# Optimization experiments

Measured on AMD Instinct MI355X. Metric: run time of the kernel, lower is better.

## Reference

```python
import jax, jax.numpy as jnp
import numpy as np

B, C, H, W = 2, 32, 256, 1216
PT = 6
EPS = 1e-6

def _conv(x, w):
    # 3x3 conv, stride 1, SAME padding, NCHW/OIHW
    return jax.lax.conv_general_dilated(x, w, (1, 1), ((1, 1), (1, 1)),
                                        dimension_numbers=('NCHW', 'OIHW', 'NCHW'))

def _cbn(x, w, s, b):
    # conv (bias=False) + eval-mode BatchNorm folded into per-channel scale/bias
    return _conv(x, w) * s[None, :, None, None] + b[None, :, None, None]

def _cb(x, w, b):
    # conv with bias (no norm branch of Basic2d)
    return _conv(x, w) + b[None, :, None, None]

def _gen_kernel(fout, w1, s1, b1, w2, s2, b2):
    # GenKernel: normalized per-pixel kernel with middle weight = 1 - sum(others)
    h = jax.nn.relu(_cbn(fout, w1, s1, b1))
    w = _cbn(h, w2, s2, b2)  # [B, pk*pk-1, H, W]
    w = w / (jnp.sum(jnp.abs(w), axis=1, keepdims=True) + EPS)
    wmid = 1.0 - jnp.sum(w, axis=1, keepdims=True)
    half = w.shape[1] // 2
    return jnp.concatenate([w[:, :half], wmid, w[:, half:]], axis=1)  # [B, pk*pk, H, W]

def _local_conv(x, w, k):
    # bpconvlocal: per-pixel spatially-varying k x k convolution of a 1-channel map
    p = k // 2
    _, _, Hx, Wx = x.shape
    xp = jnp.pad(x, ((0, 0), (0, 0), (p, p), (p, p)))
    patches = jnp.stack([xp[:, 0, i:i + Hx, j:j + Wx]
                         for i in range(k) for j in range(k)], axis=1)  # [B, k*k, H, W]
    return jnp.sum(w * patches, axis=1, keepdims=True)

def _cspn(fout, hn, h0,
          k3w1, k3s1, k3b1, k3w2, k3s2, k3b2,
          k5w1, k5s1, k5b1, k5w2, k5s2, k5b2,
          k7w1, k7s1, k7b1, k7w2, k7s2, k7b2,
          mw1, ms1, mb1, mw2, mbias2,
          cw1, cs1, cb1, cw2, cbias2,
          tw1, ts1, tb1, tw2, tbias2):
    w3 = _gen_kernel(fout, k3w1, k3s1, k3b1, k3w2, k3s2, k3b2)
    w5 = _gen_kernel(fout, k5w1, k5s1, k5b1, k5w2, k5s2, k5b2)
    w7 = _gen_kernel(fout, k7w1, k7s1, k7b1, k7w2, k7s2, k7b2)
    valid = (h0 > 0.001).astype(fout.dtype)
    mask = jax.nn.sigmoid(_cb(jax.nn.relu(_cbn(fout, mw1, ms1, mb1)), mw2, mbias2)) * valid
    m3, m5, m7 = jnp.split(mask, 3, axis=1)
    conf = jax.nn.softmax(_cb(jax.nn.relu(_cbn(fout, cw1, cs1, cb1)), cw2, cbias2), axis=1)
    c3, c5, c7 = jnp.split(conf, 3, axis=1)
    h3 = h5 = h7 = hn
    hns = [hn]
    for i in range(PT):
        h3 = (1.0 - m3) * _local_conv(h3, w3, 3) + m3 * h0
        h5 = (1.0 - m5) * _local_conv(h5, w5, 5) + m5 * h0
        h7 = (1.0 - m7) * _local_conv(h7, w7, 7) + m7 * h0
        if i == PT // 2 - 1:
            hns.append(c3 * h3 + c5 * h5 + c7 * h7)
    hns.append(c3 * h3 + c5 * h5 + c7 * h7)
    hns = jnp.concatenate(hns, axis=1)  # [B, 3, H, W]
    wt = jax.nn.softmax(_cb(jax.nn.relu(_cbn(jnp.concatenate([fout, hns], axis=1),
                                             tw1, ts1, tb1)), tw2, tbias2), axis=1)
    return jnp.sum(wt * hns, axis=1, keepdims=True)

def setup_inputs():
    key = jax.random.key(0)
    ks = iter(jax.random.split(key, 80))
    def nrm(shape, s=0.05):
        return jax.random.normal(next(ks), shape, dtype=jnp.float32) * s
    d = {}
    d['fout'] = jax.random.normal(next(ks), (B, C, H, W), dtype=jnp.float32)
    d['hn'] = jax.random.uniform(next(ks), (B, 1, H, W), dtype=jnp.float32) * 10.0
    sparse = (jax.random.uniform(next(ks), (B, 1, H, W)) < 0.06).astype(jnp.float32)
    d['h0'] = sparse * jax.random.uniform(next(ks), (B, 1, H, W), dtype=jnp.float32) * 10.0
    for pk, pre in ((3, 'k3'), (5, 'k5'), (7, 'k7')):
        co = pk * pk - 1
        d[pre + 'w1'] = nrm((C, C, 3, 3)); d[pre + 's1'] = 1.0 + nrm((C,)); d[pre + 'b1'] = nrm((C,))
        d[pre + 'w2'] = nrm((co, C, 3, 3)); d[pre + 's2'] = 1.0 + nrm((co,)); d[pre + 'b2'] = nrm((co,))
    for pre, cin in (('m', C), ('c', C), ('t', C + 3)):
        d[pre + 'w1'] = nrm((C, cin, 3, 3)); d[pre + 's1'] = 1.0 + nrm((C,)); d[pre + 'b1'] = nrm((C,))
        d[pre + 'w2'] = nrm((3, C, 3, 3)); d[pre + 'bias2'] = nrm((3,))
    return d

def reference(fout, hn, h0,
              k3w1, k3s1, k3b1, k3w2, k3s2, k3b2,
              k5w1, k5s1, k5b1, k5w2, k5s2, k5b2,
              k7w1, k7s1, k7b1, k7w2, k7s2, k7b2,
              mw1, ms1, mb1, mw2, mbias2,
              cw1, cs1, cb1, cw2, cbias2,
              tw1, ts1, tb1, tw2, tbias2):
    return _cspn(fout, hn, h0,
                 k3w1, k3s1, k3b1, k3w2, k3s2, k3b2,
                 k5w1, k5s1, k5b1, k5w2, k5s2, k5b2,
                 k7w1, k7s1, k7b1, k7w2, k7s2, k7b2,
                 mw1, ms1, mb1, mw2, mbias2,
                 cw1, cs1, cb1, cw2, cbias2,
                 tw1, ts1, tb1, tw2, tbias2)
```

## Files before the change

kernel.cpp:

```cpp
#include <hip/hip_runtime.h>
#include <hip/hip_bf16.h>

constexpr int B_ = 2, H_ = 256, W_ = 1216;
constexpr int HW = H_ * W_;
constexpr int NP = B_ * HW;
constexpr int WP = W_ + 2;
constexpr int HP = H_ + 2;
constexpr int HWP = HP * WP;
constexpr float EPS_ = 1e-6f;

constexpr int PW1_K3 = 0;
constexpr int PW1_K5 = 18432;
constexpr int PW1_K7 = 36864;
constexpr int PW2_K3 = 55296;
constexpr int PW2_K5 = 64512;
constexpr int PW2_K7 = 82944;
constexpr int PP1_M  = 110592;
constexpr int PP1_C  = 119808;
constexpr int PP1_T  = 129024;
constexpr int PP1T2  = 138240;
constexpr int PG2_M  = 140544;
constexpr int PG2_C  = 145152;
constexpr int PG2_T  = 149760;
constexpr int PREP_N = 154368;

typedef __bf16 bfrag __attribute__((ext_vector_type(8)));
typedef float f4 __attribute__((ext_vector_type(4)));

union BU { uint4 u; bfrag f; };
union U8 { uint4 u; ushort s[8]; };

__device__ __forceinline__ ushort f2b(float x) {
  uint u = __float_as_uint(x);
  u += 0x7fffu + ((u >> 16) & 1u);
  return (ushort)(u >> 16);
}
__device__ __forceinline__ float b2f(ushort u) {
  return __uint_as_float(((uint)u) << 16);
}

__global__ __launch_bounds__(256)
void prep_k(const float* __restrict__ k3w1, const float* __restrict__ k5w1,
            const float* __restrict__ k7w1, const float* __restrict__ k3w2,
            const float* __restrict__ k5w2, const float* __restrict__ k7w2,
            const float* __restrict__ mw1, const float* __restrict__ cw1,
            const float* __restrict__ tw1, const float* __restrict__ mw2,
            const float* __restrict__ cw2, const float* __restrict__ tw2,
            ushort* __restrict__ wp)
{
  int i = blockIdx.x * 256 + threadIdx.x;
  if (i >= PREP_N) return;
  ushort outv;
  if (i < PW2_K3) {
    int c = i / 18432, r = i % 18432;
    const float* src = (c == 0) ? k3w1 : (c == 1) ? k5w1 : k7w1;
    int ci = r & 31; int t1 = r >> 5;
    int co = t1 & 31; int t2 = t1 >> 5;
    int tap = t2 % 9, half = t2 / 9;
    float v = src[(co * 32 + ci) * 9 + tap];
    ushort hi = f2b(v);
    outv = half ? f2b(v - b2f(hi)) : hi;
  } else if (i < PP1_M) {
    int r = i - PW2_K3;
    const float* src; int NM16, CO;
    if (r < 9216)       { src = k3w2; NM16 = 16; CO = 8; }
    else if (r < 27648) { src = k5w2; NM16 = 32; CO = 24; r -= 9216; }
    else                { src = k7w2; NM16 = 48; CO = 48; r -= 27648; }
    int ci = r & 31; int t1 = r >> 5;
    int co = t1 % NM16; int t2 = t1 / NM16;
    int tap = t2 % 9, half = t2 / 9;
    if (co < CO) {
      float v = src[(co * 32 + ci) * 9 + tap];
      ushort hi = f2b(v);
      outv = half ? f2b(v - b2f(hi)) : hi;
    } else outv = 0;
  } else if (i < PP1T2) {
    int r = i - PP1_M;
    int c = r / 9216; r %= 9216;
    const float* src = (c == 0) ? mw1 : (c == 1) ? cw1 : tw1;
    int CIN = (c == 2) ? 35 : 32;
    int ci = r & 31; int t1 = r >> 5;
    int co = t1 & 31, tap = t1 >> 5;
    outv = f2b(src[(co * CIN + ci) * 9 + tap]);
  } else if (i < PG2_M) {
    int r = i - PP1T2;
    int c8 = r & 7; int t1 = r >> 3;
    int co = t1 & 31, tap = t1 >> 5;
    int cc = (c8 < 3) ? c8 : ((c8 < 6) ? c8 - 3 : -1);
    outv = (cc >= 0) ? f2b(tw1[(co * 35 + 32 + cc) * 9 + tap]) : (ushort)0;
  } else {
    int r = i - PG2_M;
    int c = r / 4608; r %= 4608;
    const float* src = (c == 0) ? mw2 : (c == 1) ? cw2 : tw2;
    int ci = r & 31; int t1 = r >> 5;
    int co = t1 & 15, tap = t1 >> 4;
    outv = (co < 3) ? f2b(src[(co * 32 + ci) * 9 + tap]) : (ushort)0;
  }
  wp[i] = outv;
}

__global__ __launch_bounds__(256)
void zring_k(ushort* __restrict__ hP) {
  constexpr int PB = 2 * WP * 4 + 2 * (HP - 2) * 4;
  int i = blockIdx.x * 256 + threadIdx.x;
  if (i >= 2 * PB) return;
  int b = i / PB, r = i % PB;
  size_t idx;
  if (r < WP * 4) idx = (size_t)r;
  else if (r < 2 * WP * 4) idx = (size_t)(HP - 1) * WP * 4 + (r - WP * 4);
  else {
    int q = r - 2 * WP * 4;
    int row = q >> 3, k = q & 7;
    int col = (k < 4) ? k : (WP - 1) * 4 + (k - 4);
    idx = (size_t)(row + 1) * WP * 4 + col;
  }
  *(uint4*)&hP[(size_t)b * HWP * 32 + idx * 8] = uint4{0, 0, 0, 0};
}

__global__ __launch_bounds__(256, 3)
void convs1(const float* __restrict__ xf, const ushort* __restrict__ wp,
            const float* __restrict__ scale, const float* __restrict__ bias,
            ushort* __restrict__ outh)
{
  __shared__ ushort xl[25344];

  const int tid = threadIdx.x;
  const int lane = tid & 63;
  const int wid = tid >> 6;
  const int x0 = blockIdx.x * 64, y0 = blockIdx.y * 4, b = blockIdx.z;

  for (int i = tid; i < 396 * 4; i += 256) {
    int oct = i & 3, rest = i >> 2;
    int xx = rest % 66, rr = rest / 66;
    int yy = y0 - 1 + rr, x = x0 - 1 + xx;
    uint4 vh = {0, 0, 0, 0}, vl = {0, 0, 0, 0};
    if ((unsigned)yy < (unsigned)H_ && (unsigned)x < (unsigned)W_) {
      const float* src = xf + ((size_t)b * 32 + oct * 8) * HW + (size_t)yy * W_ + x;
      uint uh[4], ul[4];
#pragma unroll
      for (int j = 0; j < 4; ++j) {
        float a = src[(size_t)(2 * j + 0) * HW];
        float c = src[(size_t)(2 * j + 1) * HW];
        ushort ah = f2b(a), ch = f2b(c);
        ushort al = f2b(a - b2f(ah)), cl = f2b(c - b2f(ch));
        uh[j] = (uint)ah | ((uint)ch << 16);
        ul[j] = (uint)al | ((uint)cl << 16);
      }
      vh = uint4{uh[0], uh[1], uh[2], uh[3]};
      vl = uint4{ul[0], ul[1], ul[2], ul[3]};
    }
    *(uint4*)&xl[rest * 32 + oct * 8] = vh;
    *(uint4*)&xl[12672 + rest * 32 + oct * 8] = vl;
  }
  __syncthreads();

  const int n = lane & 15, quad = lane >> 4;

  f4 acc[4][2];
#pragma unroll
  for (int tu = 0; tu < 4; ++tu)
#pragma unroll
    for (int mt = 0; mt < 2; ++mt) acc[tu][mt] = f4{0.f, 0.f, 0.f, 0.f};

#pragma unroll
  for (int tap = 0; tap < 9; ++tap) {
    int dy = tap / 3, dx = tap % 3;
    bfrag avhi[2], avlo[2];
#pragma unroll
    for (int mt = 0; mt < 2; ++mt) {
      avhi[mt] = *(const bfrag*)&wp[((tap * 32) + mt * 16 + n) * 32 + quad * 8];
      avlo[mt] = *(const bfrag*)&wp[(((9 + tap) * 32) + mt * 16 + n) * 32 + quad * 8];
    }
#pragma unroll
    for (int tu = 0; tu < 4; ++tu) {
      int t = wid + tu * 4;
      int r = t >> 2, g = t & 3;
      int pix = (r + dy) * 66 + g * 16 + n + dx;
      bfrag bhi = *(const bfrag*)&xl[pix * 32 + quad * 8];
      bfrag blo = *(const bfrag*)&xl[12672 + pix * 32 + quad * 8];
#pragma unroll
      for (int mt = 0; mt < 2; ++mt) {
        acc[tu][mt] = __builtin_amdgcn_mfma_f32_16x16x32_bf16(avhi[mt], bhi, acc[tu][mt], 0, 0, 0);
        acc[tu][mt] = __builtin_amdgcn_mfma_f32_16x16x32_bf16(avhi[mt], blo, acc[tu][mt], 0, 0, 0);
        acc[tu][mt] = __builtin_amdgcn_mfma_f32_16x16x32_bf16(avlo[mt], bhi, acc[tu][mt], 0, 0, 0);
      }
    }
  }

#pragma unroll
  for (int tu = 0; tu < 4; ++tu) {
    int t = wid + tu * 4;
    int r = t >> 2, g = t & 3;
    int gx = x0 + g * 16 + n, gy = y0 + r;
    size_t bpix = (size_t)b * HWP + (size_t)(gy + 1) * WP + (gx + 1);
#pragma unroll
    for (int mt = 0; mt < 2; ++mt) {
      int cob = mt * 16 + quad * 4;
      float v0 = fmaxf(acc[tu][mt][0] * scale[cob + 0] + bias[cob + 0], 0.f);
      float v1 = fmaxf(acc[tu][mt][1] * scale[cob + 1] + bias[cob + 1], 0.f);
      float v2 = fmaxf(acc[tu][mt][2] * scale[cob + 2] + bias[cob + 2], 0.f);
      float v3 = fmaxf(acc[tu][mt][3] * scale[cob + 3] + bias[cob + 3], 0.f);
      uint u0 = (uint)f2b(v0) | ((uint)f2b(v1) << 16);
      uint u1 = (uint)f2b(v2) | ((uint)f2b(v3) << 16);
      *(uint2*)&outh[bpix * 32 + cob] = uint2{u0, u1};
    }
  }
}

template<int nM, int MINW>
__global__ __launch_bounds__(256, MINW)
void convs2(const ushort* __restrict__ hP, const ushort* __restrict__ wp,
            const float* __restrict__ scale, const float* __restrict__ bias,
            ushort* __restrict__ outw, int CO)
{
  __shared__ ushort xl[12672];

  constexpr int NM16 = nM * 16;
  const int tid = threadIdx.x;
  const int lane = tid & 63;
  const int wid = tid >> 6;
  const int x0 = blockIdx.x * 64, y0 = blockIdx.y * 4, b = blockIdx.z;
  const ushort* hb = hP + (size_t)b * HWP * 32;

  for (int i = tid; i < 396 * 4; i += 256) {
    int oct = i & 3, rest = i >> 2;
    int xx = rest % 66, rr = rest / 66;
    *(uint4*)&xl[rest * 32 + oct * 8] =
        *(const uint4*)&hb[((size_t)(y0 + rr) * WP + (x0 + xx)) * 32 + oct * 8];
  }

  const int n = lane & 15, quad = lane >> 4;

  f4 acc[4][nM];
#pragma unroll
  for (int tu = 0; tu < 4; ++tu)
#pragma unroll
    for (int mt = 0; mt < nM; ++mt) acc[tu][mt] = f4{0.f, 0.f, 0.f, 0.f};

  bfrag whi[2][nM], wlo[2][nM];
#pragma unroll
  for (int mt = 0; mt < nM; ++mt) {
    whi[0][mt] = *(const bfrag*)&wp[(mt * 16 + n) * 32 + quad * 8];
    wlo[0][mt] = *(const bfrag*)&wp[((9 * NM16) + mt * 16 + n) * 32 + quad * 8];
  }
  __syncthreads();

#pragma unroll
  for (int tap = 0; tap < 9; ++tap) {
    const int dy = tap / 3, dx = tap % 3;
    const int cur = tap & 1, nxt = cur ^ 1;
    if (tap < 8) {
#pragma unroll
      for (int mt = 0; mt < nM; ++mt) {
        whi[nxt][mt] = *(const bfrag*)&wp[(((tap + 1) * NM16) + mt * 16 + n) * 32 + quad * 8];
        wlo[nxt][mt] = *(const bfrag*)&wp[(((9 + tap + 1) * NM16) + mt * 16 + n) * 32 + quad * 8];
      }
    }
#pragma unroll
    for (int tu = 0; tu < 4; ++tu) {
      int t = wid + tu * 4;
      int r = t >> 2, g = t & 3;
      int pix = (r + dy) * 66 + g * 16 + n + dx;
      bfrag bv = *(const bfrag*)&xl[pix * 32 + quad * 8];
#pragma unroll
      for (int mt = 0; mt < nM; ++mt) {
        acc[tu][mt] = __builtin_amdgcn_mfma_f32_16x16x32_bf16(whi[cur][mt], bv, acc[tu][mt], 0, 0, 0);
        acc[tu][mt] = __builtin_amdgcn_mfma_f32_16x16x32_bf16(wlo[cur][mt], bv, acc[tu][mt], 0, 0, 0);
      }
    }
  }

#pragma unroll
  for (int tu = 0; tu < 4; ++tu) {
    int t = wid + tu * 4;
    int r = t >> 2, g = t & 3;
    int gx = x0 + g * 16 + n, gy = y0 + r;
    size_t gpix = (size_t)gy * W_ + gx;

    float vs[nM][4];
    float pa = 0.f;
#pragma unroll
    for (int mt = 0; mt < nM; ++mt)
#pragma unroll
      for (int rg = 0; rg < 4; ++rg) {
        int co = mt * 16 + quad * 4 + rg;
        float v = (co < CO) ? acc[tu][mt][rg] * scale[co] + bias[co] : 0.f;
        vs[mt][rg] = v;
        pa += fabsf(v);
      }
    pa += __shfl_xor(pa, 16);
    pa += __shfl_xor(pa, 32);
    float inv = 1.f / (pa + EPS_);

    size_t base = ((size_t)b * HW + gpix) * (size_t)CO;
#pragma unroll
    for (int mt = 0; mt < nM; ++mt) {
      int cob = mt * 16 + quad * 4;
      if (cob < CO) {
        uint u0 = (uint)f2b(vs[mt][0] * inv) | ((uint)f2b(vs[mt][1] * inv) << 16);
        uint u1 = (uint)f2b(vs[mt][2] * inv) | ((uint)f2b(vs[mt][3] * inv) << 16);
        *(uint2*)&outw[base + cob] = uint2{u0, u1};
      }
    }
  }
}

template<int KB2, int MINW>
__global__ __launch_bounds__(256, MINW)
void conv1p(const float* __restrict__ xf, const float* __restrict__ hnsp,
            const ushort* __restrict__ wp, const ushort* __restrict__ wp2,
            const float* __restrict__ scale, const float* __restrict__ bias,
            ushort* __restrict__ outh)
{
  __shared__ ushort xl[396 * 32];
  __shared__ ushort xl2[KB2 ? 396 * 8 : 8];

  const int tid = threadIdx.x;
  const int lane = tid & 63;
  const int wid = tid >> 6;
  const int x0 = blockIdx.x * 64, y0 = blockIdx.y * 4, b = blockIdx.z;

  if (KB2) {
    for (int i = tid; i < 396; i += 256) {
      int xx = i % 66, rr = i / 66;
      int yy = y0 - 1 + rr, x = x0 - 1 + xx;
      float v0 = 0.f, v1 = 0.f, v2 = 0.f;
      if ((unsigned)yy < (unsigned)H_ && (unsigned)x < (unsigned)W_) {
        size_t pix = (size_t)yy * W_ + x;
        v0 = hnsp[((size_t)b * 3 + 0) * HW + pix];
        v1 = hnsp[((size_t)b * 3 + 1) * HW + pix];
        v2 = hnsp[((size_t)b * 3 + 2) * HW + pix];
      }
      ushort h0b = f2b(v0), h1b = f2b(v1), h2b = f2b(v2);
      ushort l0 = f2b(v0 - b2f(h0b)), l1 = f2b(v1 - b2f(h1b)), l2 = f2b(v2 - b2f(h2b));
      uint u0 = (uint)h0b | ((uint)h1b << 16);
      uint u1 = (uint)h2b | ((uint)l0 << 16);
      uint u2 = (uint)l1 | ((uint)l2 << 16);
      *(uint4*)&xl2[i * 8] = uint4{u0, u1, u2, 0};
    }
  }
  for (int i = tid; i < 396 * 4; i += 256) {
    int oct = i & 3, rest = i >> 2;
    int xx = rest % 66, rr = rest / 66;
    int yy = y0 - 1 + rr, x = x0 - 1 + xx;
    uint4 v = {0, 0, 0, 0};
    if ((unsigned)yy < (unsigned)H_ && (unsigned)x < (unsigned)W_) {
      const float* src = xf + ((size_t)b * 32 + oct * 8) * HW + (size_t)yy * W_ + x;
      uint u[4];
#pragma unroll
      for (int j = 0; j < 4; ++j) {
        float a = src[(size_t)(2 * j + 0) * HW];
        float c = src[(size_t)(2 * j + 1) * HW];
        u[j] = (uint)f2b(a) | ((uint)f2b(c) << 16);
      }
      v = uint4{u[0], u[1], u[2], u[3]};
    }
    *(uint4*)&xl[rest * 32 + oct * 8] = v;
  }
  __syncthreads();

  const int n = lane & 15, quad = lane >> 4;

  f4 acc[4][2];
#pragma unroll
  for (int tu = 0; tu < 4; ++tu)
#pragma unroll
    for (int mt = 0; mt < 2; ++mt) acc[tu][mt] = f4{0.f, 0.f, 0.f, 0.f};

#pragma unroll
  for (int tap = 0; tap < 9; ++tap) {
    int dy = tap / 3, dx = tap % 3;
    bfrag av[2];
#pragma unroll
    for (int mt = 0; mt < 2; ++mt)
      av[mt] = *(const bfrag*)&wp[((tap * 32) + mt * 16 + n) * 32 + quad * 8];
    bfrag a2[KB2 ? 2 : 1];
    if (KB2) {
#pragma unroll
      for (int mt = 0; mt < 2; ++mt) {
        BU t; t.u = uint4{0, 0, 0, 0};
        if (lane < 16) t.f = *(const bfrag*)&wp2[(tap * 32 + mt * 16 + lane) * 8];
        a2[mt] = t.f;
      }
    }
#pragma unroll
    for (int tu = 0; tu < 4; ++tu) {
      int t = wid + tu * 4;
      int r = t >> 2, g = t & 3;
      int pix = (r + dy) * 66 + g * 16 + n + dx;
      bfrag bv = *(const bfrag*)&xl[pix * 32 + quad * 8];
#pragma unroll
      for (int mt = 0; mt < 2; ++mt)
        acc[tu][mt] = __builtin_amdgcn_mfma_f32_16x16x32_bf16(av[mt], bv, acc[tu][mt], 0, 0, 0);
      if (KB2) {
        BU t2; t2.u = uint4{0, 0, 0, 0};
        if (lane < 16) t2.f = *(const bfrag*)&xl2[pix * 8];
#pragma unroll
        for (int mt = 0; mt < 2; ++mt)
          acc[tu][mt] = __builtin_amdgcn_mfma_f32_16x16x32_bf16(a2[mt], t2.f, acc[tu][mt], 0, 0, 0);
      }
    }
  }

#pragma unroll
  for (int tu = 0; tu < 4; ++tu) {
    int t = wid + tu * 4;
    int r = t >> 2, g = t & 3;
    int gx = x0 + g * 16 + n, gy = y0 + r;
    size_t bpix = (size_t)b * HWP + (size_t)(gy + 1) * WP + (gx + 1);
#pragma unroll
    for (int mt = 0; mt < 2; ++mt) {
      int cob = mt * 16 + quad * 4;
      float v0 = fmaxf(acc[tu][mt][0] * scale[cob + 0] + bias[cob + 0], 0.f);
      float v1 = fmaxf(acc[tu][mt][1] * scale[cob + 1] + bias[cob + 1], 0.f);
      float v2 = fmaxf(acc[tu][mt][2] * scale[cob + 2] + bias[cob + 2], 0.f);
      float v3 = fmaxf(acc[tu][mt][3] * scale[cob + 3] + bias[cob + 3], 0.f);
      uint u0 = (uint)f2b(v0) | ((uint)f2b(v1) << 16);
      uint u1 = (uint)f2b(v2) | ((uint)f2b(v3) << 16);
      *(uint2*)&outh[bpix * 32 + cob] = uint2{u0, u1};
    }
  }
}

template<int EPI>
__global__ __launch_bounds__(256, 4)
void conv2g(const ushort* __restrict__ hP, const ushort* __restrict__ wp,
            const float* __restrict__ bias, const float* __restrict__ h0,
            const float* __restrict__ hnsp, float* __restrict__ outf)
{
  __shared__ ushort xl[12672];

  const int tid = threadIdx.x;
  const int lane = tid & 63;
  const int wid = tid >> 6;
  const int x0 = blockIdx.x * 64, y0 = blockIdx.y * 4, b = blockIdx.z;
  const int n = lane & 15, quad = lane >> 4;
  const ushort* hb = hP + (size_t)b * HWP * 32;

  for (int i = tid; i < 396 * 4; i += 256) {
    int oct = i & 3, rest = i >> 2;
    int xx = rest % 66, rr = rest / 66;
    *(uint4*)&xl[rest * 32 + oct * 8] =
        *(const uint4*)&hb[((size_t)(y0 + rr) * WP + (x0 + xx)) * 32 + oct * 8];
  }

  bfrag av[9];
#pragma unroll
  for (int tap = 0; tap < 9; ++tap)
    av[tap] = *(const bfrag*)&wp[((tap * 16) + n) * 32 + quad * 8];

  f4 acc[4];
#pragma unroll
  for (int tu = 0; tu < 4; ++tu) acc[tu] = f4{0.f, 0.f, 0.f, 0.f};
  __syncthreads();

#pragma unroll
  for (int tap = 0; tap < 9; ++tap) {
    int dy = tap / 3, dx = tap % 3;
#pragma unroll
    for (int tu = 0; tu < 4; ++tu) {
      int t = wid + tu * 4;
      int r = t >> 2, g = t & 3;
      int pix = (r + dy) * 66 + g * 16 + n + dx;
      bfrag bv = *(const bfrag*)&xl[pix * 32 + quad * 8];
      acc[tu] = __builtin_amdgcn_mfma_f32_16x16x32_bf16(av[tap], bv, acc[tu], 0, 0, 0);
    }
  }

#pragma unroll
  for (int tu = 0; tu < 4; ++tu) {
    int t = wid + tu * 4;
    int r = t >> 2, g = t & 3;
    int gx = x0 + g * 16 + n, gy = y0 + r;
    size_t gpix = (size_t)gy * W_ + gx;
    size_t bpix = (size_t)b * HW + gpix;

    if constexpr (EPI == 2) {
      if (lane < 16) {
        float valid = (h0[bpix] > 0.001f) ? 1.f : 0.f;
#pragma unroll
        for (int rg = 0; rg < 3; ++rg) {
          float v = acc[tu][rg] + bias[rg];
          float sg = 1.f / (1.f + expf(-v));
          outf[((size_t)b * 3 + rg) * HW + gpix] = sg * valid;
        }
      }
    } else if constexpr (EPI == 3) {
      if (lane < 16) {
        float v0 = acc[tu][0] + bias[0];
        float v1 = acc[tu][1] + bias[1];
        float v2 = acc[tu][2] + bias[2];
        float m = fmaxf(v0, fmaxf(v1, v2));
        float e0 = expf(v0 - m), e1 = expf(v1 - m), e2 = expf(v2 - m);
        float inv = 1.f / (e0 + e1 + e2);
        outf[((size_t)b * 3 + 0) * HW + gpix] = e0 * inv;
        outf[((size_t)b * 3 + 1) * HW + gpix] = e1 * inv;
        outf[((size_t)b * 3 + 2) * HW + gpix] = e2 * inv;
      }
    } else if constexpr (EPI == 4) {
      if (lane < 16) {
        float v0 = acc[tu][0] + bias[0];
        float v1 = acc[tu][1] + bias[1];
        float v2 = acc[tu][2] + bias[2];
        float m = fmaxf(v0, fmaxf(v1, v2));
        float e0 = expf(v0 - m), e1 = expf(v1 - m), e2 = expf(v2 - m);
        float inv = 1.f / (e0 + e1 + e2);
        float a0 = hnsp[((size_t)b * 3 + 0) * HW + gpix];
        float a1 = hnsp[((size_t)b * 3 + 1) * HW + gpix];
        float a2v = hnsp[((size_t)b * 3 + 2) * HW + gpix];
        outf[bpix] = (e0 * a0 + e1 * a1 + e2 * a2v) * inv;
      }
    }
  }
}

__global__ __launch_bounds__(256)
void init_k(const float* __restrict__ hn, float* __restrict__ h3,
            float* __restrict__ h5, float* __restrict__ h7,
            float* __restrict__ hns)
{
  int t = blockIdx.x * 256 + threadIdx.x;
  if (t >= NP) return;
  float v = hn[t];
  h3[t] = v; h5[t] = v; h7[t] = v;
  int b = t / HW, rem = t - b * HW;
  hns[(size_t)b * 3 * HW + rem] = v;
}

__global__ __launch_bounds__(256)
void iterate_k(const float* __restrict__ h3i, const float* __restrict__ h5i,
               const float* __restrict__ h7i,
               float* __restrict__ h3o, float* __restrict__ h5o,
               float* __restrict__ h7o,
               const ushort* __restrict__ w3, const ushort* __restrict__ w5,
               const ushort* __restrict__ w7,
               const float* __restrict__ mask, const float* __restrict__ h0,
               float* __restrict__ hns, int chn, const float* __restrict__ conf)
{
  int t = blockIdx.x * 256 + threadIdx.x;
  if (t >= NP) return;
  int b = t / HW;
  int rem = t - b * HW;
  int y = rem / W_;
  int x = rem - y * W_;
  size_t pb = (size_t)b * HW;

  float h0v = h0[t];

  U8 a3; a3.u = *(const uint4*)&w3[((size_t)b * HW + rem) * 8];
  float s3 = 0.f, ws3 = 0.f;
#pragma unroll
  for (int p = 0; p < 8; ++p) {
    int tap = (p < 4) ? p : p + 1;
    int dy = tap / 3 - 1, dx = tap % 3 - 1;
    int yy = y + dy, xx = x + dx;
    float hv = ((unsigned)yy < (unsigned)H_ && (unsigned)xx < (unsigned)W_)
                   ? h3i[pb + yy * W_ + xx] : 0.f;
    float wv = b2f(a3.s[p]);
    ws3 += wv;
    s3 += wv * hv;
  }
  s3 += (1.f - ws3) * h3i[t];
  float m3 = mask[(size_t)(b * 3 + 0) * HW + rem];
  float n3 = (1.f - m3) * s3 + m3 * h0v;
  h3o[t] = n3;

  U8 a5[3];
  {
    const ushort* w5r = w5 + ((size_t)b * HW + rem) * 24;
#pragma unroll
    for (int q = 0; q < 3; ++q) a5[q].u = *(const uint4*)(w5r + q * 8);
  }
  float s5 = 0.f, ws5 = 0.f;
#pragma unroll
  for (int p = 0; p < 24; ++p) {
    int tap = (p < 12) ? p : p + 1;
    int dy = tap / 5 - 2, dx = tap % 5 - 2;
    int yy = y + dy, xx = x + dx;
    float hv = ((unsigned)yy < (unsigned)H_ && (unsigned)xx < (unsigned)W_)
                   ? h5i[pb + yy * W_ + xx] : 0.f;
    float wv = b2f(a5[p >> 3].s[p & 7]);
    ws5 += wv;
    s5 += wv * hv;
  }
  s5 += (1.f - ws5) * h5i[t];
  float m5 = mask[(size_t)(b * 3 + 1) * HW + rem];
  float n5 = (1.f - m5) * s5 + m5 * h0v;
  h5o[t] = n5;

  U8 a7[6];
  {
    const ushort* w7r = w7 + ((size_t)b * HW + rem) * 48;
#pragma unroll
    for (int q = 0; q < 6; ++q) a7[q].u = *(const uint4*)(w7r + q * 8);
  }
  float s7 = 0.f, ws7 = 0.f;
#pragma unroll
  for (int p = 0; p < 48; ++p) {
    int tap = (p < 24) ? p : p + 1;
    int dy = tap / 7 - 3, dx = tap % 7 - 3;
    int yy = y + dy, xx = x + dx;
    float hv = ((unsigned)yy < (unsigned)H_ && (unsigned)xx < (unsigned)W_)
                   ? h7i[pb + yy * W_ + xx] : 0.f;
    float wv = b2f(a7[p >> 3].s[p & 7]);
    ws7 += wv;
    s7 += wv * hv;
  }
  s7 += (1.f - ws7) * h7i[t];
  float m7 = mask[(size_t)(b * 3 + 2) * HW + rem];
  float n7 = (1.f - m7) * s7 + m7 * h0v;
  h7o[t] = n7;

  if (chn >= 0) {
    float c3 = conf[(size_t)(b * 3 + 0) * HW + rem];
    float c5 = conf[(size_t)(b * 3 + 1) * HW + rem];
    float c7 = conf[(size_t)(b * 3 + 2) * HW + rem];
    hns[(size_t)(b * 3 + chn) * HW + rem] = c3 * n3 + c5 * n5 + c7 * n7;
  }
}

extern "C" void kernel_launch(void* const* d_in, const int* in_sizes, int n_in,
                              void* d_out, int out_size, void* d_ws, size_t ws_size,
                              hipStream_t stream) {
  const float* fout = (const float*)d_in[0];
  const float* hn   = (const float*)d_in[1];
  const float* h0   = (const float*)d_in[2];
  const float* k3w1 = (const float*)d_in[3];
  const float* k3s1 = (const float*)d_in[4];
  const float* k3b1 = (const float*)d_in[5];
  const float* k3w2 = (const float*)d_in[6];
  const float* k3s2 = (const float*)d_in[7];
  const float* k3b2 = (const float*)d_in[8];
  const float* k5w1 = (const float*)d_in[9];
  const float* k5s1 = (const float*)d_in[10];
  const float* k5b1 = (const float*)d_in[11];
  const float* k5w2 = (const float*)d_in[12];
  const float* k5s2 = (const float*)d_in[13];
  const float* k5b2 = (const float*)d_in[14];
  const float* k7w1 = (const float*)d_in[15];
  const float* k7s1 = (const float*)d_in[16];
  const float* k7b1 = (const float*)d_in[17];
  const float* k7w2 = (const float*)d_in[18];
  const float* k7s2 = (const float*)d_in[19];
  const float* k7b2 = (const float*)d_in[20];
  const float* mw1  = (const float*)d_in[21];
  const float* ms1  = (const float*)d_in[22];
  const float* mb1  = (const float*)d_in[23];
  const float* mw2  = (const float*)d_in[24];
  const float* mbias2 = (const float*)d_in[25];
  const float* cw1  = (const float*)d_in[26];
  const float* cs1  = (const float*)d_in[27];
  const float* cb1  = (const float*)d_in[28];
  const float* cw2  = (const float*)d_in[29];
  const float* cbias2 = (const float*)d_in[30];
  const float* tw1  = (const float*)d_in[31];
  const float* ts1  = (const float*)d_in[32];
  const float* tb1  = (const float*)d_in[33];
  const float* tw2  = (const float*)d_in[34];
  const float* tbias2 = (const float*)d_in[35];

  float* out = (float*)d_out;

  size_t hP_elems = (size_t)2 * HWP * 32;
  size_t need = hP_elems * 2 + (size_t)NP * (80 * 2 + 15 * 4) + (size_t)PREP_N * 2;
  if (ws_size < need) return;
  ushort* hPb  = (ushort*)d_ws;
  ushort* w3   = hPb  + hP_elems;
  ushort* w5   = w3   + (size_t)8 * NP;
  ushort* w7   = w5   + (size_t)24 * NP;
  float* mask  = (float*)(w7 + (size_t)48 * NP);
  float* conf  = mask + (size_t)3 * NP;
  float* hA    = conf + (size_t)3 * NP;
  float* hns   = hA   + (size_t)6 * NP;
  ushort* wp   = (ushort*)(hns + (size_t)3 * NP);

  dim3 blk(256);
  dim3 gc(W_ / 64, H_ / 4, B_);
  int ge = NP / 256;
  constexpr int PB = 2 * WP * 4 + 2 * (HP - 2) * 4;
  int gz = (2 * PB + 255) / 256;
  int gp = (PREP_N + 255) / 256;

  prep_k<<<gp, blk, 0, stream>>>(k3w1, k5w1, k7w1, k3w2, k5w2, k7w2,
                                 mw1, cw1, tw1, mw2, cw2, tw2, wp);
  zring_k<<<gz, blk, 0, stream>>>(hPb);

  convs1<<<gc, blk, 0, stream>>>(fout, wp + PW1_K3, k3s1, k3b1, hPb);
  convs2<1, 4><<<gc, blk, 0, stream>>>(hPb, wp + PW2_K3, k3s2, k3b2, w3, 8);
  convs1<<<gc, blk, 0, stream>>>(fout, wp + PW1_K5, k5s1, k5b1, hPb);
  convs2<2, 4><<<gc, blk, 0, stream>>>(hPb, wp + PW2_K5, k5s2, k5b2, w5, 24);
  convs1<<<gc, blk, 0, stream>>>(fout, wp + PW1_K7, k7s1, k7b1, hPb);
  convs2<3, 3><<<gc, blk, 0, stream>>>(hPb, wp + PW2_K7, k7s2, k7b2, w7, 48);

  conv1p<0, 4><<<gc, blk, 0, stream>>>(fout, nullptr, wp + PP1_M, nullptr, ms1, mb1, hPb);
  conv2g<2><<<gc, blk, 0, stream>>>(hPb, wp + PG2_M, mbias2, h0, nullptr, mask);

  conv1p<0, 4><<<gc, blk, 0, stream>>>(fout, nullptr, wp + PP1_C, nullptr, cs1, cb1, hPb);
  conv2g<3><<<gc, blk, 0, stream>>>(hPb, wp + PG2_C, cbias2, nullptr, nullptr, conf);

  float* h3c = hA + (size_t)0 * NP; float* h3n = hA + (size_t)1 * NP;
  float* h5c = hA + (size_t)2 * NP; float* h5n = hA + (size_t)3 * NP;
  float* h7c = hA + (size_t)4 * NP; float* h7n = hA + (size_t)5 * NP;

  init_k<<<ge, blk, 0, stream>>>(hn, h3c, h5c, h7c, hns);
  for (int i = 0; i < 6; ++i) {
    int chn = (i == 2) ? 1 : ((i == 5) ? 2 : -1);
    iterate_k<<<ge, blk, 0, stream>>>(h3c, h5c, h7c, h3n, h5n, h7n,
                                      w3, w5, w7, mask, h0, hns, chn, conf);
    float* t;
    t = h3c; h3c = h3n; h3n = t;
    t = h5c; h5c = h5n; h5n = t;
    t = h7c; h7c = h7n; h7n = t;
  }

  conv1p<1, 3><<<gc, blk, 0, stream>>>(fout, hns, wp + PP1_T, wp + PP1T2, ts1, tb1, hPb);
  conv2g<4><<<gc, blk, 0, stream>>>(hPb, wp + PG2_T, tbias2, nullptr, hns, out);
}
```

Before: 899.2 us.

## Fuse first-layer convs of kernel and mask/conf branches sharing one input tile

```diff
diff --git a/kernel.cpp b/kernel.cpp
--- a/kernel.cpp
+++ b/kernel.cpp
@@ -103,8 +103,8 @@
 void zring_k(ushort* __restrict__ hP) {
   constexpr int PB = 2 * WP * 4 + 2 * (HP - 2) * 4;
   int i = blockIdx.x * 256 + threadIdx.x;
-  if (i >= 2 * PB) return;
-  int b = i / PB, r = i % PB;
+  if (i >= 6 * PB) return;
+  int bp = i / PB, r = i % PB;
   size_t idx;
   if (r < WP * 4) idx = (size_t)r;
   else if (r < 2 * WP * 4) idx = (size_t)(HP - 1) * WP * 4 + (r - WP * 4);
@@ -114,13 +114,15 @@
     int col = (k < 4) ? k : (WP - 1) * 4 + (k - 4);
     idx = (size_t)(row + 1) * WP * 4 + col;
   }
-  *(uint4*)&hP[(size_t)b * HWP * 32 + idx * 8] = uint4{0, 0, 0, 0};
+  *(uint4*)&hP[(size_t)bp * HWP * 32 + idx * 8] = uint4{0, 0, 0, 0};
 }
 
 __global__ __launch_bounds__(256, 3)
-void convs1(const float* __restrict__ xf, const ushort* __restrict__ wp,
-            const float* __restrict__ scale, const float* __restrict__ bias,
-            ushort* __restrict__ outh)
+void convs1f(const float* __restrict__ xf, const ushort* __restrict__ wp,
+             const float* __restrict__ s3, const float* __restrict__ b3,
+             const float* __restrict__ s5, const float* __restrict__ b5,
+             const float* __restrict__ s7, const float* __restrict__ b7,
+             ushort* __restrict__ outh)
 {
   __shared__ ushort xl[25344];
 
@@ -156,53 +158,165 @@
 
   const int n = lane & 15, quad = lane >> 4;
 
-  f4 acc[4][2];
-#pragma unroll
-  for (int tu = 0; tu < 4; ++tu)
-#pragma unroll
-    for (int mt = 0; mt < 2; ++mt) acc[tu][mt] = f4{0.f, 0.f, 0.f, 0.f};
-
-#pragma unroll
-  for (int tap = 0; tap < 9; ++tap) {
-    int dy = tap / 3, dx = tap % 3;
-    bfrag avhi[2], avlo[2];
+#pragma unroll 1
+  for (int br = 0; br < 3; ++br) {
+    const ushort* wb = wp + br * 18432;
+    const float* scale = (br == 0) ? s3 : (br == 1) ? s5 : s7;
+    const float* bias  = (br == 0) ? b3 : (br == 1) ? b5 : b7;
+    ushort* ob = outh + (size_t)br * 2 * HWP * 32;
+
+    f4 acc[4][2];
+#pragma unroll
+    for (int tu = 0; tu < 4; ++tu)
+#pragma unroll
+      for (int mt = 0; mt < 2; ++mt) acc[tu][mt] = f4{0.f, 0.f, 0.f, 0.f};
+
+    bfrag avhi[2][2], avlo[2][2];
 #pragma unroll
     for (int mt = 0; mt < 2; ++mt) {
-      avhi[mt] = *(const bfrag*)&wp[((tap * 32) + mt * 16 + n) * 32 + quad * 8];
-      avlo[mt] = *(const bfrag*)&wp[(((9 + tap) * 32) + mt * 16 + n) * 32 + quad * 8];
-    }
+      avhi[0][mt] = *(const bfrag*)&wb[(mt * 16 + n) * 32 + quad * 8];
+      avlo[0][mt] = *(const bfrag*)&wb[((9 * 32) + mt * 16 + n) * 32 + quad * 8];
+    }
+
+#pragma unroll
+    for (int tap = 0; tap < 9; ++tap) {
+      const int dy = tap / 3, dx = tap % 3;
+      const int cur = tap & 1, nxt = cur ^ 1;
+      if (tap < 8) {
+#pragma unroll
+        for (int mt = 0; mt < 2; ++mt) {
+          avhi[nxt][mt] = *(const bfrag*)&wb[(((tap + 1) * 32) + mt * 16 + n) * 32 + quad * 8];
+          avlo[nxt][mt] = *(const bfrag*)&wb[(((9 + tap + 1) * 32) + mt * 16 + n) * 32 + quad * 8];
+        }
+      }
+#pragma unroll
+      for (int tu = 0; tu < 4; ++tu) {
+        int t = wid + tu * 4;
+        int r = t >> 2, g = t & 3;
+        int pix = (r + dy) * 66 + g * 16 + n + dx;
+        bfrag bhi = *(const bfrag*)&xl[pix * 32 + quad * 8];
+        bfrag blo = *(const bfrag*)&xl[12672 + pix * 32 + quad * 8];
+#pragma unroll
+        for (int mt = 0; mt < 2; ++mt) {
+          acc[tu][mt] = __builtin_amdgcn_mfma_f32_16x16x32_bf16(avhi[cur][mt], bhi, acc[tu][mt], 0, 0, 0);
+          acc[tu][mt] = __builtin_amdgcn_mfma_f32_16x16x32_bf16(avhi[cur][mt], blo, acc[tu][mt], 0, 0, 0);
+          acc[tu][mt] = __builtin_amdgcn_mfma_f32_16x16x32_bf16(avlo[cur][mt], bhi, acc[tu][mt], 0, 0, 0);
+        }
+      }
+    }
+
 #pragma unroll
     for (int tu = 0; tu < 4; ++tu) {
       int t = wid + tu * 4;
       int r = t >> 2, g = t & 3;
-      int pix = (r + dy) * 66 + g * 16 + n + dx;
-      bfrag bhi = *(const bfrag*)&xl[pix * 32 + quad * 8];
-      bfrag blo = *(const bfrag*)&xl[12672 + pix * 32 + quad * 8];
+      int gx = x0 + g * 16 + n, gy = y0 + r;
+      size_t bpix = (size_t)b * HWP + (size_t)(gy + 1) * WP + (gx + 1);
 #pragma unroll
       for (int mt = 0; mt < 2; ++mt) {
-        acc[tu][mt] = __builtin_amdgcn_mfma_f32_16x16x32_bf16(avhi[mt], bhi, acc[tu][mt], 0, 0, 0);
-        acc[tu][mt] = __builtin_amdgcn_mfma_f32_16x16x32_bf16(avhi[mt], blo, acc[tu][mt], 0, 0, 0);
-        acc[tu][mt] = __builtin_amdgcn_mfma_f32_16x16x32_bf16(avlo[mt], bhi, acc[tu][mt], 0, 0, 0);
-      }
-    }
-  }
-
-#pragma unroll
-  for (int tu = 0; tu < 4; ++tu) {
-    int t = wid + tu * 4;
-    int r = t >> 2, g = t & 3;
-    int gx = x0 + g * 16 + n, gy = y0 + r;
-    size_t bpix = (size_t)b * HWP + (size_t)(gy + 1) * WP + (gx + 1);
-#pragma unroll
-    for (int mt = 0; mt < 2; ++mt) {
-      int cob = mt * 16 + quad * 4;
-      float v0 = fmaxf(acc[tu][mt][0] * scale[cob + 0] + bias[cob + 0], 0.f);
-      float v1 = fmaxf(acc[tu][mt][1] * scale[cob + 1] + bias[cob + 1], 0.f);
-      float v2 = fmaxf(acc[tu][mt][2] * scale[cob + 2] + bias[cob + 2], 0.f);
-      float v3 = fmaxf(acc[tu][mt][3] * scale[cob + 3] + bias[cob + 3], 0.f);
-      uint u0 = (uint)f2b(v0) | ((uint)f2b(v1) << 16);
-      uint u1 = (uint)f2b(v2) | ((uint)f2b(v3) << 16);
-      *(uint2*)&outh[bpix * 32 + cob] = uint2{u0, u1};
+        int cob = mt * 16 + quad * 4;
+        float v0 = fmaxf(acc[tu][mt][0] * scale[cob + 0] + bias[cob + 0], 0.f);
+        float v1 = fmaxf(acc[tu][mt][1] * scale[cob + 1] + bias[cob + 1], 0.f);
+        float v2 = fmaxf(acc[tu][mt][2] * scale[cob + 2] + bias[cob + 2], 0.f);
+        float v3 = fmaxf(acc[tu][mt][3] * scale[cob + 3] + bias[cob + 3], 0.f);
+        uint u0 = (uint)f2b(v0) | ((uint)f2b(v1) << 16);
+        uint u1 = (uint)f2b(v2) | ((uint)f2b(v3) << 16);
+        *(uint2*)&ob[bpix * 32 + cob] = uint2{u0, u1};
+      }
+    }
+  }
+}
+
+__global__ __launch_bounds__(256, 4)
+void conv1pf(const float* __restrict__ xf, const ushort* __restrict__ wp,
+             const float* __restrict__ sm, const float* __restrict__ bm,
+             const float* __restrict__ sc, const float* __restrict__ bc,
+             ushort* __restrict__ outh)
+{
+  __shared__ ushort xl[12672];
+
+  const int tid = threadIdx.x;
+  const int lane = tid & 63;
+  const int wid = tid >> 6;
+  const int x0 = blockIdx.x * 64, y0 = blockIdx.y * 4, b = blockIdx.z;
+
+  for (int i = tid; i < 396 * 4; i += 256) {
+    int oct = i & 3, rest = i >> 2;
+    int xx = rest % 66, rr = rest / 66;
+    int yy = y0 - 1 + rr, x = x0 - 1 + xx;
+    uint4 v = {0, 0, 0, 0};
+    if ((unsigned)yy < (unsigned)H_ && (unsigned)x < (unsigned)W_) {
+      const float* src = xf + ((size_t)b * 32 + oct * 8) * HW + (size_t)yy * W_ + x;
+      uint u[4];
+#pragma unroll
+      for (int j = 0; j < 4; ++j) {
+        float a = src[(size_t)(2 * j + 0) * HW];
+        float c = src[(size_t)(2 * j + 1) * HW];
+        u[j] = (uint)f2b(a) | ((uint)f2b(c) << 16);
+      }
+      v = uint4{u[0], u[1], u[2], u[3]};
+    }
+    *(uint4*)&xl[rest * 32 + oct * 8] = v;
+  }
+  __syncthreads();
+
+  const int n = lane & 15, quad = lane >> 4;
+
+#pragma unroll 1
+  for (int br = 0; br < 2; ++br) {
+    const ushort* wb = wp + br * 9216;
+    const float* scale = br ? sc : sm;
+    const float* bias  = br ? bc : bm;
+    ushort* ob = outh + (size_t)br * 2 * HWP * 32;
+
+    f4 acc[4][2];
+#pragma unroll
+    for (int tu = 0; tu < 4; ++tu)
+#pragma unroll
+      for (int mt = 0; mt < 2; ++mt) acc[tu][mt] = f4{0.f, 0.f, 0.f, 0.f};
+
+    bfrag av[2][2];
+#pragma unroll
+    for (int mt = 0; mt < 2; ++mt)
+      av[0][mt] = *(const bfrag*)&wb[(mt * 16 + n) * 32 + quad * 8];
+
+#pragma unroll
+    for (int tap = 0; tap < 9; ++tap) {
+      const int dy = tap / 3, dx = tap % 3;
+      const int cur = tap & 1, nxt = cur ^ 1;
+      if (tap < 8) {
+#pragma unroll
+        for (int mt = 0; mt < 2; ++mt)
+          av[nxt][mt] = *(const bfrag*)&wb[(((tap + 1) * 32) + mt * 16 + n) * 32 + quad * 8];
+      }
+#pragma unroll
+      for (int tu = 0; tu < 4; ++tu) {
+        int t = wid + tu * 4;
+        int r = t >> 2, g = t & 3;
+        int pix = (r + dy) * 66 + g * 16 + n + dx;
+        bfrag bv = *(const bfrag*)&xl[pix * 32 + quad * 8];
+#pragma unroll
+        for (int mt = 0; mt < 2; ++mt)
+          acc[tu][mt] = __builtin_amdgcn_mfma_f32_16x16x32_bf16(av[cur][mt], bv, acc[tu][mt], 0, 0, 0);
+      }
+    }
+
+#pragma unroll
+    for (int tu = 0; tu < 4; ++tu) {
+      int t = wid + tu * 4;
+      int r = t >> 2, g = t & 3;
+      int gx = x0 + g * 16 + n, gy = y0 + r;
+      size_t bpix = (size_t)b * HWP + (size_t)(gy + 1) * WP + (gx + 1);
+#pragma unroll
+      for (int mt = 0; mt < 2; ++mt) {
+        int cob = mt * 16 + quad * 4;
+        float v0 = fmaxf(acc[tu][mt][0] * scale[cob + 0] + bias[cob + 0], 0.f);
+        float v1 = fmaxf(acc[tu][mt][1] * scale[cob + 1] + bias[cob + 1], 0.f);
+        float v2 = fmaxf(acc[tu][mt][2] * scale[cob + 2] + bias[cob + 2], 0.f);
+        float v3 = fmaxf(acc[tu][mt][3] * scale[cob + 3] + bias[cob + 3], 0.f);
+        uint u0 = (uint)f2b(v0) | ((uint)f2b(v1) << 16);
+        uint u1 = (uint)f2b(v2) | ((uint)f2b(v3) << 16);
+        *(uint2*)&ob[bpix * 32 + cob] = uint2{u0, u1};
+      }
     }
   }
 }
@@ -662,10 +776,10 @@
   float* out = (float*)d_out;
 
   size_t hP_elems = (size_t)2 * HWP * 32;
-  size_t need = hP_elems * 2 + (size_t)NP * (80 * 2 + 15 * 4) + (size_t)PREP_N * 2;
+  size_t need = hP_elems * 3 * 2 + (size_t)NP * (80 * 2 + 15 * 4) + (size_t)PREP_N * 2;
   if (ws_size < need) return;
   ushort* hPb  = (ushort*)d_ws;
-  ushort* w3   = hPb  + hP_elems;
+  ushort* w3   = hPb  + 3 * hP_elems;
   ushort* w5   = w3   + (size_t)8 * NP;
   ushort* w7   = w5   + (size_t)24 * NP;
   float* mask  = (float*)(w7 + (size_t)48 * NP);
@@ -678,25 +792,22 @@
   dim3 gc(W_ / 64, H_ / 4, B_);
   int ge = NP / 256;
   constexpr int PB = 2 * WP * 4 + 2 * (HP - 2) * 4;
-  int gz = (2 * PB + 255) / 256;
+  int gz = (6 * PB + 255) / 256;
   int gp = (PREP_N + 255) / 256;
 
   prep_k<<<gp, blk, 0, stream>>>(k3w1, k5w1, k7w1, k3w2, k5w2, k7w2,
                                  mw1, cw1, tw1, mw2, cw2, tw2, wp);
   zring_k<<<gz, blk, 0, stream>>>(hPb);
 
-  convs1<<<gc, blk, 0, stream>>>(fout, wp + PW1_K3, k3s1, k3b1, hPb);
-  convs2<1, 4><<<gc, blk, 0, stream>>>(hPb, wp + PW2_K3, k3s2, k3b2, w3, 8);
-  convs1<<<gc, blk, 0, stream>>>(fout, wp + PW1_K5, k5s1, k5b1, hPb);
-  convs2<2, 4><<<gc, blk, 0, stream>>>(hPb, wp + PW2_K5, k5s2, k5b2, w5, 24);
-  convs1<<<gc, blk, 0, stream>>>(fout, wp + PW1_K7, k7s1, k7b1, hPb);
-  convs2<3, 3><<<gc, blk, 0, stream>>>(hPb, wp + PW2_K7, k7s2, k7b2, w7, 48);
-
-  conv1p<0, 4><<<gc, blk, 0, stream>>>(fout, nullptr, wp + PP1_M, nullptr, ms1, mb1, hPb);
-  conv2g<2><<<gc, blk, 0, stream>>>(hPb, wp + PG2_M, mbias2, h0, nullptr, mask);
-
-  conv1p<0, 4><<<gc, blk, 0, stream>>>(fout, nullptr, wp + PP1_C, nullptr, cs1, cb1, hPb);
-  conv2g<3><<<gc, blk, 0, stream>>>(hPb, wp + PG2_C, cbias2, nullptr, nullptr, conf);
+  convs1f<<<gc, blk, 0, stream>>>(fout, wp + PW1_K3,
+                                  k3s1, k3b1, k5s1, k5b1, k7s1, k7b1, hPb);
+  convs2<1, 4><<<gc, blk, 0, stream>>>(hPb,                 wp + PW2_K3, k3s2, k3b2, w3, 8);
+  convs2<2, 4><<<gc, blk, 0, stream>>>(hPb + hP_elems,      wp + PW2_K5, k5s2, k5b2, w5, 24);
+  convs2<3, 3><<<gc, blk, 0, stream>>>(hPb + 2 * hP_elems,  wp + PW2_K7, k7s2, k7b2, w7, 48);
+
+  conv1pf<<<gc, blk, 0, stream>>>(fout, wp + PP1_M, ms1, mb1, cs1, cb1, hPb);
+  conv2g<2><<<gc, blk, 0, stream>>>(hPb,            wp + PG2_M, mbias2, h0, nullptr, mask);
+  conv2g<3><<<gc, blk, 0, stream>>>(hPb + hP_elems, wp + PG2_C, cbias2, nullptr, nullptr, conf);
 
   float* h3c = hA + (size_t)0 * NP; float* h3n = hA + (size_t)1 * NP;
   float* h5c = hA + (size_t)2 * NP; float* h5n = hA + (size_t)3 * NP;
```

Result: slower. 951.4 us (+5.8%).
